# Performance work log

Measured on AMD Instinct MI355X. Metric: run time of the kernel, lower is better.

## Reference

```python
import jax, jax.numpy as jnp
import numpy as np

B, T, N, FI, FO = 4, 8, 1024, 64, 64
ALPHA = 0.2          # LeakyReLU negative slope
NEG_INF = -1e12      # matches torch's -1000000000000.0


def setup_inputs() -> dict:
    key = jax.random.key(0)
    k0, k1, k2, k3, k4 = jax.random.split(key, 5)
    inp = jax.random.normal(k0, (B, T, N, FI), dtype=jnp.float32)
    u = jax.random.uniform(k1, (T, N, N), dtype=jnp.float32)
    adj = jnp.where(u > 0.9, u, 0.0)
    # att_mask: [batch, node, seq] in {0,1}
    att_mask = (jax.random.uniform(k2, (B, N, T)) > 0.2).astype(jnp.float32)
    # xavier-ish init (gain 1.414)
    W = jax.random.normal(k3, (FI, FO), dtype=jnp.float32) * (1.414 * np.sqrt(2.0 / (FI + FO)))
    a = jax.random.normal(k4, (2 * FO, 1), dtype=jnp.float32) * (1.414 * np.sqrt(2.0 / (2 * FO + 1)))
    return {"adj": adj, "inp": inp, "att_mask": att_mask, "W": W, "a": a}


def reference(adj, inp, att_mask, W, a):
    Fo = W.shape[1]
    h = jnp.einsum('btnf,fo->btno', inp, W)               # [B,T,N,Fo]
    # additive decomposition of a^T [h_i || h_j] = a1.h_i + a2.h_j
    a1 = a[:Fo, 0]
    a2 = a[Fo:, 0]
    s1 = jnp.einsum('btno,o->btn', h, a1)                 # contributes along rows (i)
    s2 = jnp.einsum('btno,o->btn', h, a2)                 # contributes along cols (j)
    e = s1[..., :, None] + s2[..., None, :]               # [B,T,N,N]
    e = jnp.where(e > 0, e, ALPHA * e)                    # LeakyReLU
    att = jnp.where(adj > 0, e * adj, NEG_INF)            # adj broadcasts over batch
    att = jax.nn.softmax(att, axis=-1)
    m = jnp.transpose(att_mask, (0, 2, 1))                # [B,T,N]
    att = att * (m[..., :, None] * m[..., None, :])       # outer-product mask
    # dropout is identity in eval mode
    h_prime = jnp.einsum('btij,btjo->btio', att, h)       # [B,T,N,Fo]
    return jax.nn.elu(h_prime)                            # concat=True path
```

## Files before the change

### kernel.cpp

```cpp
#include <hip/hip_runtime.h>
#include <hip/hip_bf16.h>
#include <math.h>

#define N_NODES 1024
#define T_DIM 8

typedef __bf16 bf16x8 __attribute__((ext_vector_type(8)));
typedef float  f32x4  __attribute__((ext_vector_type(4)));

__device__ __forceinline__ float readlane_f(float v, int l) {
    return __uint_as_float(__builtin_amdgcn_readlane(__float_as_uint(v), l));
}

__global__ __launch_bounds__(256) void gat_h_kernel(
    const float* __restrict__ inp, const float* __restrict__ W,
    const float* __restrict__ a, const float* __restrict__ att_mask,
    __bf16* __restrict__ hT, float* __restrict__ s1w, float* __restrict__ s2w)
{
    __shared__ float Wl[64 * 64];
    __shared__ float xl[64 * 64];
    __shared__ __bf16 htl[64 * 66];

    const int tid  = threadIdx.x;
    const int blk  = blockIdx.x;
    const int bt   = blk >> 4;
    const int b    = bt >> 3;
    const int t    = bt & 7;
    const int n0   = (blk & 15) * 64;
    const int lane = tid & 63;
    const int wave = tid >> 6;

    const float4* W4  = (const float4*)W;
    float4*       Wl4 = (float4*)Wl;
    const float4* x4  = (const float4*)(inp + (size_t)(bt * N_NODES + n0) * 64);
    float4*       xl4 = (float4*)xl;
#pragma unroll
    for (int k = 0; k < 4; ++k) {
        Wl4[tid + k * 256] = W4[tid + k * 256];
        xl4[tid + k * 256] = x4[tid + k * 256];
    }
    const float a1 = a[lane];
    const float a2 = a[64 + lane];
    __syncthreads();

#pragma unroll 1
    for (int rg = 0; rg < 16; rg += 4) {
        float xr[4], acc[4];
#pragma unroll
        for (int q = 0; q < 4; ++q) {
            xr[q]  = xl[(wave * 16 + rg + q) * 64 + lane];
            acc[q] = 0.f;
        }
#pragma unroll
        for (int f = 0; f < 64; ++f) {
            float w = Wl[f * 64 + lane];
#pragma unroll
            for (int q = 0; q < 4; ++q)
                acc[q] = fmaf(readlane_f(xr[q], f), w, acc[q]);
        }
#pragma unroll
        for (int q = 0; q < 4; ++q) {
            const int r = wave * 16 + rg + q;
            float v1 = acc[q] * a1, v2 = acc[q] * a2;
#pragma unroll
            for (int off = 32; off; off >>= 1) {
                v1 += __shfl_xor(v1, off, 64);
                v2 += __shfl_xor(v2, off, 64);
            }
            if (lane == 0) {
                s1w[bt * N_NODES + n0 + r] = v1;
                s2w[bt * N_NODES + n0 + r] = v2;
            }
            const float mjr = att_mask[((size_t)b * N_NODES + n0 + r) * T_DIM + t];
            htl[lane * 66 + r] = (__bf16)(acc[q] * mjr);
        }
    }
    __syncthreads();

    {
        const int o  = tid >> 2;
        const int r0 = (tid & 3) * 16;
        unsigned u[8];
#pragma unroll
        for (int k = 0; k < 8; ++k)
            u[k] = *(const unsigned*)&htl[o * 66 + r0 + 2 * k];
        uint4* dst = (uint4*)(hT + (size_t)(bt * 64 + o) * N_NODES + n0 + r0);
        dst[0] = make_uint4(u[0], u[1], u[2], u[3]);
        dst[1] = make_uint4(u[4], u[5], u[6], u[7]);
    }
}

__global__ __launch_bounds__(64) void gat_attn_kernel(
    const float* __restrict__ adj, const float* __restrict__ att_mask,
    const __bf16* __restrict__ hT, const float* __restrict__ s1w,
    const float* __restrict__ s2w, float* __restrict__ out)
{
    __shared__ __align__(16) __bf16 p_l[16 * 72];

    const int bt    = blockIdx.y;
    const int b     = bt >> 3;
    const int t     = bt & 7;
    const int irow0 = blockIdx.x * 16;
    const int lane  = threadIdx.x;

    f32x4 acc[4];
#pragma unroll
    for (int nc = 0; nc < 4; ++nc) acc[nc] = (f32x4){0.f, 0.f, 0.f, 0.f};
    float lsum[16], s1v[16];
#pragma unroll
    for (int r = 0; r < 16; ++r) {
        lsum[r] = 0.f;
        s1v[r]  = s1w[bt * N_NODES + irow0 + r];
    }

    const float*  adjrow = adj + (size_t)t * N_NODES * N_NODES
                               + (size_t)irow0 * N_NODES + lane;
    const __bf16* hlane  = hT + (size_t)bt * 64 * N_NODES
                              + (size_t)(lane & 15) * N_NODES + (lane >> 4) * 8;
    const float*  s2bt   = s2w + bt * N_NODES;
    __bf16* pwr = p_l + lane;
    const __bf16* prd = p_l + (lane & 15) * 72 + (lane >> 4) * 8;

    float  adj0[16], adj1[16];
    bf16x8 hc[8];
    float  s2c;
#pragma unroll
    for (int r = 0; r < 16; ++r) {
        adj0[r] = adjrow[(size_t)r * N_NODES];
        adj1[r] = adjrow[(size_t)r * N_NODES + 64];
    }
#pragma unroll
    for (int kc = 0; kc < 2; ++kc)
#pragma unroll
        for (int nc = 0; nc < 4; ++nc)
            hc[kc * 4 + nc] = *(const bf16x8*)(hlane + (size_t)nc * 16 * N_NODES + kc * 32);
    s2c = s2bt[lane];

#pragma unroll
    for (int it = 0; it < 16; ++it) {
        const int j2 = (it < 14) ? (it + 2) * 64 : 0;
        const int j1 = (it < 15) ? (it + 1) * 64 : 0;
        float  adjn[16];
        bf16x8 hn[8];
#pragma unroll
        for (int r = 0; r < 16; ++r) adjn[r] = adjrow[(size_t)r * N_NODES + j2];
#pragma unroll
        for (int kc = 0; kc < 2; ++kc)
#pragma unroll
            for (int nc = 0; nc < 4; ++nc)
                hn[kc * 4 + nc] = *(const bf16x8*)(hlane + (size_t)nc * 16 * N_NODES + j1 + kc * 32);
        const float s2n = s2bt[j1 + lane];

#pragma unroll
        for (int r = 0; r < 16; ++r) {
            float e = s1v[r] + s2c;
            e = (e > 0.f) ? e : 0.2f * e;
            float p = (adj0[r] > 0.f) ? __expf(e * adj0[r]) : 0.f;
            lsum[r] += p;
            pwr[r * 72] = (__bf16)p;
        }

        bf16x8 af0 = *(const bf16x8*)(prd);
        bf16x8 af1 = *(const bf16x8*)(prd + 32);
#pragma unroll
        for (int nc = 0; nc < 4; ++nc)
            acc[nc] = __builtin_amdgcn_mfma_f32_16x16x32_bf16(af0, hc[nc], acc[nc], 0, 0, 0);
#pragma unroll
        for (int nc = 0; nc < 4; ++nc)
            acc[nc] = __builtin_amdgcn_mfma_f32_16x16x32_bf16(af1, hc[4 + nc], acc[nc], 0, 0, 0);

#pragma unroll
        for (int r = 0; r < 16; ++r) { adj0[r] = adj1[r]; adj1[r] = adjn[r]; }
#pragma unroll
        for (int k = 0; k < 8; ++k) hc[k] = hn[k];
        s2c = s2n;
    }

#pragma unroll
    for (int r = 0; r < 16; ++r) {
#pragma unroll
        for (int off = 32; off; off >>= 1)
            lsum[r] += __shfl_xor(lsum[r], off, 64);
    }
    const int q = lane >> 4;
#pragma unroll
    for (int reg = 0; reg < 4; ++reg) {
        float ls = (q == 0) ? lsum[reg] : (q == 1) ? lsum[4 + reg]
                 : (q == 2) ? lsum[8 + reg] : lsum[12 + reg];
        const int i = irow0 + q * 4 + reg;
        float mi    = att_mask[((size_t)b * N_NODES + i) * T_DIM + t];
        float scale = mi / ls;
#pragma unroll
        for (int nc = 0; nc < 4; ++nc) {
            float v = acc[nc][reg] * scale;
            v = (v > 0.f) ? v : (__expf(v) - 1.f);
            out[((size_t)bt * N_NODES + i) * 64 + nc * 16 + (lane & 15)] = v;
        }
    }
}

extern "C" void kernel_launch(void* const* d_in, const int* in_sizes, int n_in,
                              void* d_out, int out_size, void* d_ws, size_t ws_size,
                              hipStream_t stream) {
    (void)in_sizes; (void)n_in; (void)out_size; (void)ws_size;
    const float* adj      = (const float*)d_in[0];
    const float* inp      = (const float*)d_in[1];
    const float* att_mask = (const float*)d_in[2];
    const float* W        = (const float*)d_in[3];
    const float* a        = (const float*)d_in[4];
    float* out = (float*)d_out;

    __bf16* hT  = (__bf16*)d_ws;
    float*  s1w = (float*)((char*)d_ws + (size_t)4 * 1024 * 1024);
    float*  s2w = s1w + 32 * N_NODES;

    gat_h_kernel<<<512, 256, 0, stream>>>(inp, W, a, att_mask, hT, s1w, s2w);
    dim3 grid(64, 32);
    gat_attn_kernel<<<grid, 64, 0, stream>>>(adj, att_mask, hT, s1w, s2w, out);
}
```

Measured before the change: 146.0 us.

## Compute attention probabilities directly in MFMA A-operand layout, drop LDS staging

Each lane now computes the softmax numerators for exactly the row and column positions it feeds into the MFMA A operand, loading adj and s2 as float4 vectors, so the shared-memory round trip for P is removed. Row sums are reduced with two cross-lane shuffles instead of sixteen full-wave reductions. Prefetch depth drops from two tiles to one and the main loop is only partly unrolled. Each lane also now loads its own s2 values instead of sharing them through broadcast. Memory latency hiding may suffer because of the shallower prefetch.

```diff
diff --git a/kernel.cpp b/kernel.cpp
--- a/kernel.cpp
+++ b/kernel.cpp
@@ -95,106 +95,102 @@
     const __bf16* __restrict__ hT, const float* __restrict__ s1w,
     const float* __restrict__ s2w, float* __restrict__ out)
 {
-    __shared__ __align__(16) __bf16 p_l[16 * 72];
-
     const int bt    = blockIdx.y;
     const int b     = bt >> 3;
     const int t     = bt & 7;
     const int irow0 = blockIdx.x * 16;
     const int lane  = threadIdx.x;
+    const int l15   = lane & 15;
+    const int quad  = lane >> 4;
 
     f32x4 acc[4];
 #pragma unroll
     for (int nc = 0; nc < 4; ++nc) acc[nc] = (f32x4){0.f, 0.f, 0.f, 0.f};
-    float lsum[16], s1v[16];
-#pragma unroll
-    for (int r = 0; r < 16; ++r) {
-        lsum[r] = 0.f;
-        s1v[r]  = s1w[bt * N_NODES + irow0 + r];
-    }
-
-    const float*  adjrow = adj + (size_t)t * N_NODES * N_NODES
-                               + (size_t)irow0 * N_NODES + lane;
-    const __bf16* hlane  = hT + (size_t)bt * 64 * N_NODES
-                              + (size_t)(lane & 15) * N_NODES + (lane >> 4) * 8;
-    const float*  s2bt   = s2w + bt * N_NODES;
-    __bf16* pwr = p_l + lane;
-    const __bf16* prd = p_l + (lane & 15) * 72 + (lane >> 4) * 8;
-
-    float  adj0[16], adj1[16];
+    float lsum = 0.f;
+    const float s1r = s1w[bt * N_NODES + irow0 + l15];
+
+    const float*  adjp  = adj + (size_t)t * N_NODES * N_NODES
+                              + (size_t)(irow0 + l15) * N_NODES + quad * 8;
+    const __bf16* hlane = hT + (size_t)bt * 64 * N_NODES
+                             + (size_t)l15 * N_NODES + quad * 8;
+    const float*  s2p   = s2w + bt * N_NODES + quad * 8;
+
+    float4 adjc[4], s2c[4];
     bf16x8 hc[8];
-    float  s2c;
-#pragma unroll
-    for (int r = 0; r < 16; ++r) {
-        adj0[r] = adjrow[(size_t)r * N_NODES];
-        adj1[r] = adjrow[(size_t)r * N_NODES + 64];
+#pragma unroll
+    for (int k = 0; k < 2; ++k) {
+        adjc[k]     = *(const float4*)(adjp + k * 4);
+        adjc[2 + k] = *(const float4*)(adjp + 32 + k * 4);
+        s2c[k]      = *(const float4*)(s2p + k * 4);
+        s2c[2 + k]  = *(const float4*)(s2p + 32 + k * 4);
     }
 #pragma unroll
     for (int kc = 0; kc < 2; ++kc)
 #pragma unroll
         for (int nc = 0; nc < 4; ++nc)
             hc[kc * 4 + nc] = *(const bf16x8*)(hlane + (size_t)nc * 16 * N_NODES + kc * 32);
-    s2c = s2bt[lane];
-
-#pragma unroll
+
+#pragma unroll 2
     for (int it = 0; it < 16; ++it) {
-        const int j2 = (it < 14) ? (it + 2) * 64 : 0;
         const int j1 = (it < 15) ? (it + 1) * 64 : 0;
-        float  adjn[16];
+
+        float4 adjn[4], s2n[4];
         bf16x8 hn[8];
 #pragma unroll
-        for (int r = 0; r < 16; ++r) adjn[r] = adjrow[(size_t)r * N_NODES + j2];
+        for (int k = 0; k < 2; ++k) {
+            adjn[k]     = *(const float4*)(adjp + j1 + k * 4);
+            adjn[2 + k] = *(const float4*)(adjp + j1 + 32 + k * 4);
+            s2n[k]      = *(const float4*)(s2p + j1 + k * 4);
+            s2n[2 + k]  = *(const float4*)(s2p + j1 + 32 + k * 4);
+        }
 #pragma unroll
         for (int kc = 0; kc < 2; ++kc)
 #pragma unroll
             for (int nc = 0; nc < 4; ++nc)
                 hn[kc * 4 + nc] = *(const bf16x8*)(hlane + (size_t)nc * 16 * N_NODES + j1 + kc * 32);
-        const float s2n = s2bt[j1 + lane];
-
-#pragma unroll
-        for (int r = 0; r < 16; ++r) {
-            float e = s1v[r] + s2c;
-            e = (e > 0.f) ? e : 0.2f * e;
-            float p = (adj0[r] > 0.f) ? __expf(e * adj0[r]) : 0.f;
-            lsum[r] += p;
-            pwr[r * 72] = (__bf16)p;
-        }
-
-        bf16x8 af0 = *(const bf16x8*)(prd);
-        bf16x8 af1 = *(const bf16x8*)(prd + 32);
+
+        const float* ac = (const float*)adjc;
+        const float* sc = (const float*)s2c;
+        bf16x8 af[2];
+#pragma unroll
+        for (int kc = 0; kc < 2; ++kc)
+#pragma unroll
+            for (int m = 0; m < 8; ++m) {
+                float av = ac[kc * 8 + m];
+                float e  = s1r + sc[kc * 8 + m];
+                e = fmaxf(e, 0.2f * e);
+                float p = (av > 0.f) ? __expf(e * av) : 0.f;
+                lsum += p;
+                af[kc][m] = (__bf16)p;
+            }
+
 #pragma unroll
         for (int nc = 0; nc < 4; ++nc)
-            acc[nc] = __builtin_amdgcn_mfma_f32_16x16x32_bf16(af0, hc[nc], acc[nc], 0, 0, 0);
+            acc[nc] = __builtin_amdgcn_mfma_f32_16x16x32_bf16(af[0], hc[nc], acc[nc], 0, 0, 0);
 #pragma unroll
         for (int nc = 0; nc < 4; ++nc)
-            acc[nc] = __builtin_amdgcn_mfma_f32_16x16x32_bf16(af1, hc[4 + nc], acc[nc], 0, 0, 0);
-
-#pragma unroll
-        for (int r = 0; r < 16; ++r) { adj0[r] = adj1[r]; adj1[r] = adjn[r]; }
+            acc[nc] = __builtin_amdgcn_mfma_f32_16x16x32_bf16(af[1], hc[4 + nc], acc[nc], 0, 0, 0);
+
+#pragma unroll
+        for (int k = 0; k < 4; ++k) { adjc[k] = adjn[k]; s2c[k] = s2n[k]; }
 #pragma unroll
         for (int k = 0; k < 8; ++k) hc[k] = hn[k];
-        s2c = s2n;
-    }
-
-#pragma unroll
-    for (int r = 0; r < 16; ++r) {
-#pragma unroll
-        for (int off = 32; off; off >>= 1)
-            lsum[r] += __shfl_xor(lsum[r], off, 64);
-    }
-    const int q = lane >> 4;
+    }
+
+    lsum += __shfl_xor(lsum, 16, 64);
+    lsum += __shfl_xor(lsum, 32, 64);
+
 #pragma unroll
     for (int reg = 0; reg < 4; ++reg) {
-        float ls = (q == 0) ? lsum[reg] : (q == 1) ? lsum[4 + reg]
-                 : (q == 2) ? lsum[8 + reg] : lsum[12 + reg];
-        const int i = irow0 + q * 4 + reg;
-        float mi    = att_mask[((size_t)b * N_NODES + i) * T_DIM + t];
+        const int i = irow0 + quad * 4 + reg;
+        float ls = __shfl(lsum, quad * 4 + reg, 64);
+        float mi = att_mask[((size_t)b * N_NODES + i) * T_DIM + t];
         float scale = mi / ls;
 #pragma unroll
         for (int nc = 0; nc < 4; ++nc) {
             float v = acc[nc][reg] * scale;
             v = (v > 0.f) ? v : (__expf(v) - 1.f);
-            out[((size_t)bt * N_NODES + i) * 64 + nc * 16 + (lane & 15)] = v;
+            out[((size_t)bt * N_NODES + i) * 64 + nc * 16 + l15] = v;
         }
     }
 }
```

After: 149.6 us. +2.5%, slower.

## Store h in swizzled contiguous tiles and stage B fragments through LDS

Applied to the files above, without the earlier changes.

The projection kernel now writes hT as contiguous 64x64 bf16 tiles per (bt, node-tile), with an XOR swizzle on 16-byte groups. The attention kernel then loads each tile with fully coalesced 16-byte-per-lane reads, stores it into shared memory, and reads MFMA B fragments back through the swizzled layout to avoid bank conflicts. It also cuts adj prefetch depth from two tiles to one and unrolls the main loop by 2 instead of fully, lowering register pressure. The cost is an extra LDS round-trip per tile and a shorter prefetch distance for adj, which could expose global memory latency. Reusing htile each iteration without a barrier is safe only because the block is a single wave.

```diff
diff --git a/kernel.cpp b/kernel.cpp
--- a/kernel.cpp
+++ b/kernel.cpp
@@ -26,7 +26,8 @@
     const int bt   = blk >> 4;
     const int b    = bt >> 3;
     const int t    = bt & 7;
-    const int n0   = (blk & 15) * 64;
+    const int nt   = blk & 15;
+    const int n0   = nt * 64;
     const int lane = tid & 63;
     const int wave = tid >> 6;
 
@@ -80,13 +81,15 @@
     {
         const int o  = tid >> 2;
         const int r0 = (tid & 3) * 16;
+        const int s  = o & 7;
         unsigned u[8];
 #pragma unroll
         for (int k = 0; k < 8; ++k)
             u[k] = *(const unsigned*)&htl[o * 66 + r0 + 2 * k];
-        uint4* dst = (uint4*)(hT + (size_t)(bt * 64 + o) * N_NODES + n0 + r0);
-        dst[0] = make_uint4(u[0], u[1], u[2], u[3]);
-        dst[1] = make_uint4(u[4], u[5], u[6], u[7]);
+        __bf16* tbase = hT + ((size_t)(bt * 16 + nt) * 64 + o) * 64;
+        const int g0 = (r0 >> 3);
+        *(uint4*)(tbase + ((g0    ) ^ s) * 8) = make_uint4(u[0], u[1], u[2], u[3]);
+        *(uint4*)(tbase + ((g0 | 1) ^ s) * 8) = make_uint4(u[4], u[5], u[6], u[7]);
     }
 }
 
@@ -95,6 +98,7 @@
     const __bf16* __restrict__ hT, const float* __restrict__ s1w,
     const float* __restrict__ s2w, float* __restrict__ out)
 {
+    __shared__ __align__(16) __bf16 htile[64 * 64];
     __shared__ __align__(16) __bf16 p_l[16 * 72];
 
     const int bt    = blockIdx.y;
@@ -102,6 +106,8 @@
     const int t     = bt & 7;
     const int irow0 = blockIdx.x * 16;
     const int lane  = threadIdx.x;
+    const int l15   = lane & 15;
+    const int quad  = lane >> 4;
 
     f32x4 acc[4];
 #pragma unroll
@@ -115,64 +121,72 @@
 
     const float*  adjrow = adj + (size_t)t * N_NODES * N_NODES
                                + (size_t)irow0 * N_NODES + lane;
-    const __bf16* hlane  = hT + (size_t)bt * 64 * N_NODES
-                              + (size_t)(lane & 15) * N_NODES + (lane >> 4) * 8;
+    const char*   tb     = (const char*)(hT + (size_t)bt * 16 * 4096);
     const float*  s2bt   = s2w + bt * N_NODES;
     __bf16* pwr = p_l + lane;
-    const __bf16* prd = p_l + (lane & 15) * 72 + (lane >> 4) * 8;
-
-    float  adj0[16], adj1[16];
-    bf16x8 hc[8];
-    float  s2c;
-#pragma unroll
-    for (int r = 0; r < 16; ++r) {
-        adj0[r] = adjrow[(size_t)r * N_NODES];
-        adj1[r] = adjrow[(size_t)r * N_NODES + 64];
-    }
-#pragma unroll
-    for (int kc = 0; kc < 2; ++kc)
-#pragma unroll
-        for (int nc = 0; nc < 4; ++nc)
-            hc[kc * 4 + nc] = *(const bf16x8*)(hlane + (size_t)nc * 16 * N_NODES + kc * 32);
+    const __bf16* prd = p_l + l15 * 72 + quad * 8;
+    const int swz = l15 & 7;
+
+    uint4 hreg[8];
+    float adjc[16];
+    float s2c;
+#pragma unroll
+    for (int c = 0; c < 8; ++c)
+        hreg[c] = *(const uint4*)(tb + c * 1024 + lane * 16);
+#pragma unroll
+    for (int r = 0; r < 16; ++r) adjc[r] = adjrow[(size_t)r * N_NODES];
     s2c = s2bt[lane];
 
-#pragma unroll
+#pragma unroll 2
     for (int it = 0; it < 16; ++it) {
-        const int j2 = (it < 14) ? (it + 2) * 64 : 0;
-        const int j1 = (it < 15) ? (it + 1) * 64 : 0;
-        float  adjn[16];
-        bf16x8 hn[8];
-#pragma unroll
-        for (int r = 0; r < 16; ++r) adjn[r] = adjrow[(size_t)r * N_NODES + j2];
-#pragma unroll
-        for (int kc = 0; kc < 2; ++kc)
-#pragma unroll
-            for (int nc = 0; nc < 4; ++nc)
-                hn[kc * 4 + nc] = *(const bf16x8*)(hlane + (size_t)nc * 16 * N_NODES + j1 + kc * 32);
-        const float s2n = s2bt[j1 + lane];
+        const int jn = (it < 15) ? (it + 1) * 64 : 0;
+        const char* tbn = tb + (size_t)(jn >> 6) * 8192;
+
+        uint4 hregn[8];
+        float adjn[16];
+#pragma unroll
+        for (int c = 0; c < 8; ++c)
+            hregn[c] = *(const uint4*)(tbn + c * 1024 + lane * 16);
+#pragma unroll
+        for (int r = 0; r < 16; ++r) adjn[r] = adjrow[(size_t)r * N_NODES + jn];
+        const float s2n = s2bt[jn + lane];
+
+#pragma unroll
+        for (int c = 0; c < 8; ++c)
+            *(uint4*)((char*)htile + c * 1024 + lane * 16) = hreg[c];
 
 #pragma unroll
         for (int r = 0; r < 16; ++r) {
             float e = s1v[r] + s2c;
-            e = (e > 0.f) ? e : 0.2f * e;
-            float p = (adj0[r] > 0.f) ? __expf(e * adj0[r]) : 0.f;
+            e = fmaxf(e, 0.2f * e);
+            float p = (adjc[r] > 0.f) ? __expf(e * adjc[r]) : 0.f;
             lsum[r] += p;
             pwr[r * 72] = (__bf16)p;
         }
 
         bf16x8 af0 = *(const bf16x8*)(prd);
         bf16x8 af1 = *(const bf16x8*)(prd + 32);
+        bf16x8 bfr[8];
+#pragma unroll
+        for (int kc = 0; kc < 2; ++kc)
+#pragma unroll
+            for (int nc = 0; nc < 4; ++nc) {
+                const int o = nc * 16 + l15;
+                const int g = (kc * 4 + quad) ^ swz;
+                bfr[kc * 4 + nc] = *(const bf16x8*)&htile[o * 64 + g * 8];
+            }
+
 #pragma unroll
         for (int nc = 0; nc < 4; ++nc)
-            acc[nc] = __builtin_amdgcn_mfma_f32_16x16x32_bf16(af0, hc[nc], acc[nc], 0, 0, 0);
+            acc[nc] = __builtin_amdgcn_mfma_f32_16x16x32_bf16(af0, bfr[nc], acc[nc], 0, 0, 0);
 #pragma unroll
         for (int nc = 0; nc < 4; ++nc)
-            acc[nc] = __builtin_amdgcn_mfma_f32_16x16x32_bf16(af1, hc[4 + nc], acc[nc], 0, 0, 0);
-
-#pragma unroll
-        for (int r = 0; r < 16; ++r) { adj0[r] = adj1[r]; adj1[r] = adjn[r]; }
-#pragma unroll
-        for (int k = 0; k < 8; ++k) hc[k] = hn[k];
+            acc[nc] = __builtin_amdgcn_mfma_f32_16x16x32_bf16(af1, bfr[4 + nc], acc[nc], 0, 0, 0);
+
+#pragma unroll
+        for (int c = 0; c < 8; ++c) hreg[c] = hregn[c];
+#pragma unroll
+        for (int r = 0; r < 16; ++r) adjc[r] = adjn[r];
         s2c = s2n;
     }
 
@@ -182,19 +196,18 @@
         for (int off = 32; off; off >>= 1)
             lsum[r] += __shfl_xor(lsum[r], off, 64);
     }
-    const int q = lane >> 4;
 #pragma unroll
     for (int reg = 0; reg < 4; ++reg) {
-        float ls = (q == 0) ? lsum[reg] : (q == 1) ? lsum[4 + reg]
-                 : (q == 2) ? lsum[8 + reg] : lsum[12 + reg];
-        const int i = irow0 + q * 4 + reg;
+        float ls = (quad == 0) ? lsum[reg] : (quad == 1) ? lsum[4 + reg]
+                 : (quad == 2) ? lsum[8 + reg] : lsum[12 + reg];
+        const int i = irow0 + quad * 4 + reg;
         float mi    = att_mask[((size_t)b * N_NODES + i) * T_DIM + t];
         float scale = mi / ls;
 #pragma unroll
         for (int nc = 0; nc < 4; ++nc) {
             float v = acc[nc][reg] * scale;
             v = (v > 0.f) ? v : (__expf(v) - 1.f);
-            out[((size_t)bt * N_NODES + i) * 64 + nc * 16 + (lane & 15)] = v;
+            out[((size_t)bt * N_NODES + i) * 64 + nc * 16 + l15] = v;
         }
     }
 }
```

After: 195.4 us. 1.34x slower.
